# Optimization experiments

Measured on AMD Instinct MI355X. Metric: run time of the kernel, lower is better.

Reference implementation:

```python
import jax, jax.numpy as jnp
import numpy as np

N_NODES = 100000
N_EDGES = 3200000
F_IN = 128
F_OUT = 128


def setup_inputs() -> dict:
    key = jax.random.key(0)
    k_x, k_r, k_c, k_v, k_w = jax.random.split(key, 5)
    x = jax.random.normal(k_x, (N_NODES, F_IN), dtype=jnp.float32)
    adj_rows = jnp.sort(jax.random.randint(k_r, (N_EDGES,), 0, N_NODES, dtype=jnp.int32))
    adj_cols = jax.random.randint(k_c, (N_EDGES,), 0, N_NODES, dtype=jnp.int32)
    adj_vals = jax.random.uniform(k_v, (N_EDGES,), dtype=jnp.float32)
    # glorot init for W, zeros for bias (as in the original module)
    limit = np.sqrt(6.0 / (F_IN + F_OUT)).astype(np.float32)
    W = jax.random.uniform(k_w, (F_IN, F_OUT), dtype=jnp.float32, minval=-limit, maxval=limit)
    b = jnp.zeros((F_OUT,), dtype=jnp.float32)
    return {"x": x, "adj_rows": adj_rows, "adj_cols": adj_cols,
            "adj_vals": adj_vals, "W": W, "b": b}


def reference(x, adj_rows, adj_cols, adj_vals, W, b):
    # dropout = 0.0 (disabled), sparse_inputs = False, featureless = False
    # pre_sup = x @ W  -- dense feature transform [N, F_out]
    pre_sup = jnp.matmul(x, W)
    # support @ pre_sup -- sparse adjacency SpMM via gather + segment_sum
    msgs = adj_vals[:, None] * pre_sup[adj_cols]        # [E, F_out]
    agg = jax.ops.segment_sum(msgs, adj_rows,
                              num_segments=N_NODES,
                              indices_are_sorted=True)   # [N, F_out]
    out = agg + b
    return jax.nn.relu(out)
```

## Files before the change

kernel.cpp:

```cpp
#include <hip/hip_runtime.h>
#include <cstdint>
#include <cstddef>

#define N_NODES 100000
#define N_EDGES 3200000
#define F_IN 128
#define F_OUT 128
#define KPAD 136

#define ROWPTR_BYTES ((N_NODES + 1) * 4)
#define O_XB   (((ROWPTR_BYTES) + 255) & ~255)
#define XB_BYTES (N_NODES * F_IN * 2)
#define O_AXB  (O_XB + XB_BYTES)
#define AXB_BYTES (N_NODES * F_OUT * 2)
#define O_WT_A (O_AXB + AXB_BYTES)
#define WT_LIN_BYTES (F_OUT * F_IN * 2)
#define NEED_A ((size_t)(O_WT_A + WT_LIN_BYTES))
#define O_WT_A2 O_AXB
#define WT_KPAD_BYTES (F_OUT * KPAD * 2)
#define NEED_A2 ((size_t)(O_WT_A2 + WT_KPAD_BYTES))
#define O_WT_B O_XB
#define NEED_B ((size_t)(O_WT_B + WT_KPAD_BYTES))

typedef __attribute__((ext_vector_type(8))) short short8;
typedef __attribute__((ext_vector_type(4))) float f32x4;

__device__ __forceinline__ unsigned short f2bf(float f) {
    union { float f; unsigned u; } v; v.f = f;
    return (unsigned short)((v.u + 0x7FFFu + ((v.u >> 16) & 1u)) >> 16);
}
__device__ __forceinline__ float bflo(unsigned u) {
    union { unsigned u; float f; } v; v.u = u << 16; return v.f;
}
__device__ __forceinline__ float bfhi(unsigned u) {
    union { unsigned u; float f; } v; v.u = u & 0xFFFF0000u; return v.f;
}

__device__ __forceinline__ int lower_bound_i32(const int* __restrict__ a, int n, int key) {
    int lo = 0, hi = n;
    while (lo < hi) {
        int mid = (lo + hi) >> 1;
        if (a[mid] < key) lo = mid + 1; else hi = mid;
    }
    return lo;
}

__global__ __launch_bounds__(256) void build_rowptr_kernel(
    const int* __restrict__ rows, int* __restrict__ rowptr)
{
    const int n = blockIdx.x * 256 + threadIdx.x;
    if (n <= N_NODES) rowptr[n] = lower_bound_i32(rows, N_EDGES, n);
}

__global__ __launch_bounds__(256) void convert_x_kernel(
    const float4* __restrict__ x4, uint2* __restrict__ xb2)
{
    const unsigned i = blockIdx.x * 256 + threadIdx.x;
    if (i < (N_NODES * F_IN / 4)) {
        const float4 a = x4[i];
        uint2 p;
        p.x = (unsigned)f2bf(a.x) | ((unsigned)f2bf(a.y) << 16);
        p.y = (unsigned)f2bf(a.z) | ((unsigned)f2bf(a.w) << 16);
        xb2[i] = p;
    }
}

__global__ __launch_bounds__(256) void build_wt_lin_kernel(
    const float* __restrict__ W, unsigned short* __restrict__ Wt)
{
    const int idx = blockIdx.x * 256 + threadIdx.x;
    if (idx < F_IN * F_OUT) {
        const int c = idx >> 7, k = idx & 127;
        Wt[idx] = f2bf(W[k * F_OUT + c]);
    }
}

__global__ __launch_bounds__(256) void build_wt_kpad_kernel(
    const float* __restrict__ W, unsigned short* __restrict__ Wt)
{
    const int idx = blockIdx.x * 256 + threadIdx.x;
    if (idx < F_IN * F_OUT) {
        const int c = idx >> 7, k = idx & 127;
        Wt[c * KPAD + k] = f2bf(W[k * F_OUT + c]);
    }
}

template<int OUT_MODE>
__global__ __launch_bounds__(256) void spmm_xb_kernel(
    const unsigned* __restrict__ xb,
    const int*      __restrict__ cols,
    const float*    __restrict__ vals,
    const int*      __restrict__ rowptr,
    void*           __restrict__ outp)
{
    const int row  = blockIdx.x * 4 + (threadIdx.x >> 6);
    const int lane = threadIdx.x & 63;
    if (row >= N_NODES) return;

    const int e0 = rowptr[row], e1 = rowptr[row + 1];
    float ax = 0.f, ay = 0.f;

    int e = e0;
    for (; e + 16 <= e1; e += 16) {
        int c[16]; float v[16]; unsigned u[16];
        #pragma unroll
        for (int j = 0; j < 16; ++j) { c[j] = cols[e + j]; v[j] = vals[e + j]; }
        #pragma unroll
        for (int j = 0; j < 16; ++j) u[j] = xb[(unsigned)c[j] * 64u + lane];
        #pragma unroll
        for (int j = 0; j < 16; ++j) {
            ax = fmaf(v[j], bflo(u[j]), ax);
            ay = fmaf(v[j], bfhi(u[j]), ay);
        }
    }
    for (; e + 4 <= e1; e += 4) {
        int c[4]; float v[4]; unsigned u[4];
        #pragma unroll
        for (int j = 0; j < 4; ++j) { c[j] = cols[e + j]; v[j] = vals[e + j]; }
        #pragma unroll
        for (int j = 0; j < 4; ++j) u[j] = xb[(unsigned)c[j] * 64u + lane];
        #pragma unroll
        for (int j = 0; j < 4; ++j) {
            ax = fmaf(v[j], bflo(u[j]), ax);
            ay = fmaf(v[j], bfhi(u[j]), ay);
        }
    }
    for (; e < e1; ++e) {
        const float v = vals[e];
        const unsigned u = xb[(unsigned)cols[e] * 64u + lane];
        ax = fmaf(v, bflo(u), ax);
        ay = fmaf(v, bfhi(u), ay);
    }

    if (OUT_MODE == 0) {
        float2 o; o.x = ax; o.y = ay;
        reinterpret_cast<float2*>(outp)[(size_t)row * 64 + lane] = o;
    } else {
        const unsigned p = (unsigned)f2bf(ax) | ((unsigned)f2bf(ay) << 16);
        reinterpret_cast<unsigned*>(outp)[(size_t)row * 64 + lane] = p;
    }
}

__global__ __launch_bounds__(256) void gemm_direct_mfma(
    const unsigned short* __restrict__ AXb,
    const unsigned short* __restrict__ Wt,
    const float*          __restrict__ bias,
    float*                __restrict__ out)
{
    const int t    = threadIdx.x;
    const int lane = t & 63;
    const int w    = t >> 6;
    const int lr   = lane & 15;
    const int lg   = lane >> 4;
    const int row0 = blockIdx.x * 64 + w * 16;

    const short* __restrict__ Arow =
        reinterpret_cast<const short*>(AXb) + (size_t)(row0 + lr) * F_IN + lg * 8;
    const short* __restrict__ Wbase =
        reinterpret_cast<const short*>(Wt) + lr * F_IN + lg * 8;

    f32x4 acc[8];
    #pragma unroll
    for (int n = 0; n < 8; ++n) acc[n] = (f32x4){0.f, 0.f, 0.f, 0.f};

    #pragma unroll
    for (int ks = 0; ks < 4; ++ks) {
        const short8 a = *reinterpret_cast<const short8*>(Arow + ks * 32);
        #pragma unroll
        for (int n = 0; n < 8; ++n) {
            const short8 b = *reinterpret_cast<const short8*>(
                Wbase + n * 16 * F_IN + ks * 32);
            acc[n] = __builtin_amdgcn_mfma_f32_16x16x32_bf16(a, b, acc[n], 0, 0, 0);
        }
    }

    const int row_base = row0 + lg * 4;
    #pragma unroll
    for (int n = 0; n < 8; ++n) {
        const int col = n * 16 + lr;
        const float bb = bias[col];
        #pragma unroll
        for (int reg = 0; reg < 4; ++reg) {
            const int r = row_base + reg;
            if (r < N_NODES)
                out[(size_t)r * F_OUT + col] = fmaxf(acc[n][reg] + bb, 0.f);
        }
    }
}

template<bool USE_ROWPTR>
__global__ __launch_bounds__(256) void spmm_ax_kernel(
    const float* __restrict__ x,
    const int*   __restrict__ rows,
    const int*   __restrict__ cols,
    const float* __restrict__ vals,
    const int*   __restrict__ rowptr,
    float*       __restrict__ out)
{
    const int row  = blockIdx.x * 4 + (threadIdx.x >> 6);
    const int lane = threadIdx.x & 63;
    if (row >= N_NODES) return;
    int e0, e1;
    if (USE_ROWPTR) { e0 = rowptr[row]; e1 = rowptr[row + 1]; }
    else {
        e0 = lower_bound_i32(rows, N_EDGES, row);
        e1 = lower_bound_i32(rows, N_EDGES, row + 1);
    }
    const float2* __restrict__ x2 = reinterpret_cast<const float2*>(x);
    float ax = 0.f, ay = 0.f;
    int e = e0;
    for (; e + 8 <= e1; e += 8) {
        int c[8]; float v[8]; float2 a[8];
        #pragma unroll
        for (int j = 0; j < 8; ++j) { c[j] = cols[e + j]; v[j] = vals[e + j]; }
        #pragma unroll
        for (int j = 0; j < 8; ++j) a[j] = x2[(unsigned)c[j] * 64u + lane];
        #pragma unroll
        for (int j = 0; j < 8; ++j) {
            ax = fmaf(v[j], a[j].x, ax); ay = fmaf(v[j], a[j].y, ay);
        }
    }
    for (; e < e1; ++e) {
        const float v = vals[e];
        const float2 a = x2[(unsigned)cols[e] * 64u + lane];
        ax = fmaf(v, a.x, ax); ay = fmaf(v, a.y, ay);
    }
    float2 o; o.x = ax; o.y = ay;
    reinterpret_cast<float2*>(out)[(size_t)row * 64 + lane] = o;
}

template<bool WT_WS>
__global__ __launch_bounds__(256) void gemm_mfma_bias_relu_inplace(
    float*                __restrict__ out,
    const unsigned short* __restrict__ Wt_ws,
    const float*          __restrict__ W,
    const float*          __restrict__ bias)
{
    __shared__ short A_lds[64][KPAD];
    __shared__ short Wt_lds[F_OUT][KPAD];
    const int t  = threadIdx.x;
    const int r0 = blockIdx.x * 64;
    const int rows_here = (N_NODES - r0 < 64) ? (N_NODES - r0) : 64;
    {
        const float4* __restrict__ A4 =
            reinterpret_cast<const float4*>(out + (size_t)r0 * F_IN);
        const int nA = rows_here * 32;
        for (int i = t; i < nA; i += 256) {
            const int r = i >> 5, q = i & 31;
            const float4 va = A4[i];
            uint2 p;
            p.x = (unsigned)f2bf(va.x) | ((unsigned)f2bf(va.y) << 16);
            p.y = (unsigned)f2bf(va.z) | ((unsigned)f2bf(va.w) << 16);
            *reinterpret_cast<uint2*>(&A_lds[r][q * 4]) = p;
        }
    }
    if (WT_WS) {
        const float4* __restrict__ src = reinterpret_cast<const float4*>(Wt_ws);
        float4* dst = reinterpret_cast<float4*>(&Wt_lds[0][0]);
        for (int i = t; i < (WT_KPAD_BYTES / 16); i += 256) dst[i] = src[i];
    } else {
        if (t < F_OUT)
            for (int k = 0; k < F_IN; ++k)
                Wt_lds[t][k] = (short)f2bf(W[k * F_OUT + t]);
    }
    __syncthreads();

    const int lane = t & 63, w = t >> 6, lr = lane & 15, lg = lane >> 4;
    f32x4 acc[8];
    #pragma unroll
    for (int n = 0; n < 8; ++n) acc[n] = (f32x4){0.f, 0.f, 0.f, 0.f};
    #pragma unroll
    for (int ks = 0; ks < 4; ++ks) {
        const short8 a = *reinterpret_cast<const short8*>(
            &A_lds[w * 16 + lr][ks * 32 + lg * 8]);
        #pragma unroll
        for (int n = 0; n < 8; ++n) {
            const short8 b = *reinterpret_cast<const short8*>(
                &Wt_lds[n * 16 + lr][ks * 32 + lg * 8]);
            acc[n] = __builtin_amdgcn_mfma_f32_16x16x32_bf16(a, b, acc[n], 0, 0, 0);
        }
    }
    const int row_base = r0 + w * 16 + lg * 4;
    #pragma unroll
    for (int n = 0; n < 8; ++n) {
        const int col = n * 16 + lr;
        const float bb = bias[col];
        #pragma unroll
        for (int reg = 0; reg < 4; ++reg) {
            const int r = row_base + reg;
            if (r < N_NODES)
                out[(size_t)r * F_OUT + col] = fmaxf(acc[n][reg] + bb, 0.f);
        }
    }
}

extern "C" void kernel_launch(void* const* d_in, const int* in_sizes, int n_in,
                              void* d_out, int out_size, void* d_ws, size_t ws_size,
                              hipStream_t stream) {
    const float* x    = (const float*)d_in[0];
    const int*   rows = (const int*)  d_in[1];
    const int*   cols = (const int*)  d_in[2];
    const float* vals = (const float*)d_in[3];
    const float* W    = (const float*)d_in[4];
    const float* b    = (const float*)d_in[5];
    float* out = (float*)d_out;
    char*  ws  = (char*)d_ws;

    if (ws_size >= NEED_A) {
        int* rowptr = (int*)ws;
        unsigned short* xb  = (unsigned short*)(ws + O_XB);
        unsigned short* AXb = (unsigned short*)(ws + O_AXB);
        unsigned short* Wt  = (unsigned short*)(ws + O_WT_A);
        build_rowptr_kernel<<<(N_NODES + 256) / 256, 256, 0, stream>>>(rows, rowptr);
        convert_x_kernel<<<(N_NODES * F_IN / 4 + 255) / 256, 256, 0, stream>>>(
            (const float4*)x, (uint2*)xb);
        build_wt_lin_kernel<<<(F_IN * F_OUT + 255) / 256, 256, 0, stream>>>(W, Wt);
        spmm_xb_kernel<1><<<(N_NODES + 3) / 4, 256, 0, stream>>>(
            (const unsigned*)xb, cols, vals, rowptr, AXb);
        gemm_direct_mfma<<<(N_NODES + 63) / 64, 256, 0, stream>>>(AXb, Wt, b, out);
    } else if (ws_size >= NEED_A2) {
        int* rowptr = (int*)ws;
        unsigned short* xb = (unsigned short*)(ws + O_XB);
        unsigned short* Wt = (unsigned short*)(ws + O_WT_A2);
        build_rowptr_kernel<<<(N_NODES + 256) / 256, 256, 0, stream>>>(rows, rowptr);
        convert_x_kernel<<<(N_NODES * F_IN / 4 + 255) / 256, 256, 0, stream>>>(
            (const float4*)x, (uint2*)xb);
        build_wt_kpad_kernel<<<(F_IN * F_OUT + 255) / 256, 256, 0, stream>>>(W, Wt);
        spmm_xb_kernel<0><<<(N_NODES + 3) / 4, 256, 0, stream>>>(
            (const unsigned*)xb, cols, vals, rowptr, out);
        gemm_mfma_bias_relu_inplace<true><<<(N_NODES + 63) / 64, 256, 0, stream>>>(
            out, Wt, nullptr, b);
    } else if (ws_size >= NEED_B) {
        int* rowptr = (int*)ws;
        unsigned short* Wt = (unsigned short*)(ws + O_WT_B);
        build_rowptr_kernel<<<(N_NODES + 256) / 256, 256, 0, stream>>>(rows, rowptr);
        build_wt_kpad_kernel<<<(F_IN * F_OUT + 255) / 256, 256, 0, stream>>>(W, Wt);
        spmm_ax_kernel<true><<<(N_NODES + 3) / 4, 256, 0, stream>>>(
            x, rows, cols, vals, rowptr, out);
        gemm_mfma_bias_relu_inplace<true><<<(N_NODES + 63) / 64, 256, 0, stream>>>(
            out, Wt, nullptr, b);
    } else {
        spmm_ax_kernel<false><<<(N_NODES + 3) / 4, 256, 0, stream>>>(
            x, rows, cols, vals, nullptr, out);
        gemm_mfma_bias_relu_inplace<false><<<(N_NODES + 63) / 64, 256, 0, stream>>>(
            out, nullptr, W, b);
    }
}
```

Baseline: 283.8 us.

## Fuse SpMM into MFMA GEMM via LDS and merge prep kernels

Merges the rowptr build, x-to-bf16 conversion and W transpose into one prep kernel. The SpMM and GEMM are fused so each block aggregates 64 rows into swizzled LDS and then runs the MFMA GEMM with bias and ReLU directly. This removes the bf16 AX intermediate round trip through global memory and several launches. In exchange the grid drops from 25000 blocks to about 1563, each wave processing 16 rows serially, which reduces parallelism and latency hiding for the gather-bound SpMM.

```diff
diff --git a/kernel.cpp b/kernel.cpp
--- a/kernel.cpp
+++ b/kernel.cpp
@@ -6,21 +6,13 @@
 #define N_EDGES 3200000
 #define F_IN 128
 #define F_OUT 128
-#define KPAD 136
 
 #define ROWPTR_BYTES ((N_NODES + 1) * 4)
 #define O_XB   (((ROWPTR_BYTES) + 255) & ~255)
 #define XB_BYTES (N_NODES * F_IN * 2)
-#define O_AXB  (O_XB + XB_BYTES)
-#define AXB_BYTES (N_NODES * F_OUT * 2)
-#define O_WT_A (O_AXB + AXB_BYTES)
-#define WT_LIN_BYTES (F_OUT * F_IN * 2)
-#define NEED_A ((size_t)(O_WT_A + WT_LIN_BYTES))
-#define O_WT_A2 O_AXB
-#define WT_KPAD_BYTES (F_OUT * KPAD * 2)
-#define NEED_A2 ((size_t)(O_WT_A2 + WT_KPAD_BYTES))
-#define O_WT_B O_XB
-#define NEED_B ((size_t)(O_WT_B + WT_KPAD_BYTES))
+#define O_WT   (O_XB + XB_BYTES)
+#define WT_BYTES (F_OUT * F_IN * 2)
+#define NEED_A ((size_t)(O_WT + WT_BYTES))
 
 typedef __attribute__((ext_vector_type(8))) short short8;
 typedef __attribute__((ext_vector_type(4))) float f32x4;
@@ -45,119 +37,99 @@
     return lo;
 }
 
-__global__ __launch_bounds__(256) void build_rowptr_kernel(
-    const int* __restrict__ rows, int* __restrict__ rowptr)
-{
-    const int n = blockIdx.x * 256 + threadIdx.x;
-    if (n <= N_NODES) rowptr[n] = lower_bound_i32(rows, N_EDGES, n);
-}
-
-__global__ __launch_bounds__(256) void convert_x_kernel(
-    const float4* __restrict__ x4, uint2* __restrict__ xb2)
-{
-    const unsigned i = blockIdx.x * 256 + threadIdx.x;
-    if (i < (N_NODES * F_IN / 4)) {
-        const float4 a = x4[i];
+__global__ __launch_bounds__(256) void prep_kernel(
+    const float*    __restrict__ x4_,
+    const int*      __restrict__ rows,
+    const float*    __restrict__ W,
+    int*            __restrict__ rowptr,
+    uint2*          __restrict__ xb2,
+    unsigned short* __restrict__ Wt)
+{
+    const unsigned g = blockIdx.x * 256 + threadIdx.x;
+    const float4* __restrict__ x4 = (const float4*)x4_;
+
+    if (g < (N_NODES * F_IN / 4)) {
+        const float4 a = x4[g];
         uint2 p;
         p.x = (unsigned)f2bf(a.x) | ((unsigned)f2bf(a.y) << 16);
         p.y = (unsigned)f2bf(a.z) | ((unsigned)f2bf(a.w) << 16);
-        xb2[i] = p;
-    }
-}
-
-__global__ __launch_bounds__(256) void build_wt_lin_kernel(
-    const float* __restrict__ W, unsigned short* __restrict__ Wt)
-{
-    const int idx = blockIdx.x * 256 + threadIdx.x;
-    if (idx < F_IN * F_OUT) {
-        const int c = idx >> 7, k = idx & 127;
-        Wt[idx] = f2bf(W[k * F_OUT + c]);
-    }
-}
-
-__global__ __launch_bounds__(256) void build_wt_kpad_kernel(
-    const float* __restrict__ W, unsigned short* __restrict__ Wt)
-{
-    const int idx = blockIdx.x * 256 + threadIdx.x;
-    if (idx < F_IN * F_OUT) {
-        const int c = idx >> 7, k = idx & 127;
-        Wt[c * KPAD + k] = f2bf(W[k * F_OUT + c]);
-    }
-}
-
-template<int OUT_MODE>
-__global__ __launch_bounds__(256) void spmm_xb_kernel(
-    const unsigned* __restrict__ xb,
-    const int*      __restrict__ cols,
-    const float*    __restrict__ vals,
-    const int*      __restrict__ rowptr,
-    void*           __restrict__ outp)
-{
-    const int row  = blockIdx.x * 4 + (threadIdx.x >> 6);
-    const int lane = threadIdx.x & 63;
-    if (row >= N_NODES) return;
-
-    const int e0 = rowptr[row], e1 = rowptr[row + 1];
-    float ax = 0.f, ay = 0.f;
-
-    int e = e0;
-    for (; e + 16 <= e1; e += 16) {
-        int c[16]; float v[16]; unsigned u[16];
-        #pragma unroll
-        for (int j = 0; j < 16; ++j) { c[j] = cols[e + j]; v[j] = vals[e + j]; }
-        #pragma unroll
-        for (int j = 0; j < 16; ++j) u[j] = xb[(unsigned)c[j] * 64u + lane];
-        #pragma unroll
-        for (int j = 0; j < 16; ++j) {
-            ax = fmaf(v[j], bflo(u[j]), ax);
-            ay = fmaf(v[j], bfhi(u[j]), ay);
-        }
-    }
-    for (; e + 4 <= e1; e += 4) {
-        int c[4]; float v[4]; unsigned u[4];
-        #pragma unroll
-        for (int j = 0; j < 4; ++j) { c[j] = cols[e + j]; v[j] = vals[e + j]; }
-        #pragma unroll
-        for (int j = 0; j < 4; ++j) u[j] = xb[(unsigned)c[j] * 64u + lane];
-        #pragma unroll
-        for (int j = 0; j < 4; ++j) {
-            ax = fmaf(v[j], bflo(u[j]), ax);
-            ay = fmaf(v[j], bfhi(u[j]), ay);
-        }
-    }
-    for (; e < e1; ++e) {
-        const float v = vals[e];
-        const unsigned u = xb[(unsigned)cols[e] * 64u + lane];
-        ax = fmaf(v, bflo(u), ax);
-        ay = fmaf(v, bfhi(u), ay);
-    }
-
-    if (OUT_MODE == 0) {
-        float2 o; o.x = ax; o.y = ay;
-        reinterpret_cast<float2*>(outp)[(size_t)row * 64 + lane] = o;
-    } else {
-        const unsigned p = (unsigned)f2bf(ax) | ((unsigned)f2bf(ay) << 16);
-        reinterpret_cast<unsigned*>(outp)[(size_t)row * 64 + lane] = p;
-    }
-}
-
-__global__ __launch_bounds__(256) void gemm_direct_mfma(
-    const unsigned short* __restrict__ AXb,
+        xb2[g] = p;
+    }
+    if (g <= N_NODES)
+        rowptr[g] = lower_bound_i32(rows, N_EDGES, g);
+    if (g < F_IN * F_OUT) {
+        const int c = g >> 7, k = g & 127;
+        Wt[g] = f2bf(W[k * F_OUT + c]);
+    }
+}
+
+__global__ __launch_bounds__(256) void fused_spmm_gemm(
+    const unsigned*       __restrict__ xb,
+    const int*            __restrict__ cols,
+    const float*          __restrict__ vals,
+    const int*            __restrict__ rowptr,
     const unsigned short* __restrict__ Wt,
     const float*          __restrict__ bias,
     float*                __restrict__ out)
 {
+    __shared__ char A_lds[64 * 256];
+
     const int t    = threadIdx.x;
     const int lane = t & 63;
     const int w    = t >> 6;
-    const int lr   = lane & 15;
-    const int lg   = lane >> 4;
-    const int row0 = blockIdx.x * 64 + w * 16;
-
-    const short* __restrict__ Arow =
-        reinterpret_cast<const short*>(AXb) + (size_t)(row0 + lr) * F_IN + lg * 8;
+    const int r0   = blockIdx.x * 64;
+
+    for (int i = 0; i < 16; ++i) {
+        const int lrow = w * 16 + i;
+        const int row  = r0 + lrow;
+        float ax = 0.f, ay = 0.f;
+        if (row < N_NODES) {
+            const int e0 = rowptr[row], e1 = rowptr[row + 1];
+            int e = e0;
+            for (; e + 16 <= e1; e += 16) {
+                int c[16]; float v[16]; unsigned u[16];
+                #pragma unroll
+                for (int j = 0; j < 16; ++j) { c[j] = cols[e + j]; v[j] = vals[e + j]; }
+                #pragma unroll
+                for (int j = 0; j < 16; ++j) u[j] = xb[(unsigned)c[j] * 64u + lane];
+                #pragma unroll
+                for (int j = 0; j < 16; ++j) {
+                    ax = fmaf(v[j], bflo(u[j]), ax);
+                    ay = fmaf(v[j], bfhi(u[j]), ay);
+                }
+            }
+            for (; e + 4 <= e1; e += 4) {
+                int c[4]; float v[4]; unsigned u[4];
+                #pragma unroll
+                for (int j = 0; j < 4; ++j) { c[j] = cols[e + j]; v[j] = vals[e + j]; }
+                #pragma unroll
+                for (int j = 0; j < 4; ++j) u[j] = xb[(unsigned)c[j] * 64u + lane];
+                #pragma unroll
+                for (int j = 0; j < 4; ++j) {
+                    ax = fmaf(v[j], bflo(u[j]), ax);
+                    ay = fmaf(v[j], bfhi(u[j]), ay);
+                }
+            }
+            for (; e < e1; ++e) {
+                const float v = vals[e];
+                const unsigned u = xb[(unsigned)cols[e] * 64u + lane];
+                ax = fmaf(v, bflo(u), ax);
+                ay = fmaf(v, bfhi(u), ay);
+            }
+        }
+        const unsigned p = (unsigned)f2bf(ax) | ((unsigned)f2bf(ay) << 16);
+        *reinterpret_cast<unsigned*>(
+            A_lds + lrow * 256 + ((lane * 4) ^ ((lrow & 7) << 4))) = p;
+    }
+    __syncthreads();
+
+    const int lr = lane & 15;
+    const int lg = lane >> 4;
+    const int swA = (lr & 7) << 4;
+
     const short* __restrict__ Wbase =
         reinterpret_cast<const short*>(Wt) + lr * F_IN + lg * 8;
+    const char* Abase = A_lds + (w * 16 + lr) * 256;
 
     f32x4 acc[8];
     #pragma unroll
@@ -165,7 +137,8 @@
 
     #pragma unroll
     for (int ks = 0; ks < 4; ++ks) {
-        const short8 a = *reinterpret_cast<const short8*>(Arow + ks * 32);
+        const short8 a = *reinterpret_cast<const short8*>(
+            Abase + ((ks * 64 + lg * 16) ^ swA));
         #pragma unroll
         for (int n = 0; n < 8; ++n) {
             const short8 b = *reinterpret_cast<const short8*>(
@@ -174,7 +147,7 @@
         }
     }
 
-    const int row_base = row0 + lg * 4;
+    const int row_base = r0 + w * 16 + lg * 4;
     #pragma unroll
     for (int n = 0; n < 8; ++n) {
         const int col = n * 16 + lr;
@@ -188,24 +161,18 @@
     }
 }
 
-template<bool USE_ROWPTR>
-__global__ __launch_bounds__(256) void spmm_ax_kernel(
+__global__ __launch_bounds__(256) void spmm_ax_fallback(
     const float* __restrict__ x,
     const int*   __restrict__ rows,
     const int*   __restrict__ cols,
     const float* __restrict__ vals,
-    const int*   __restrict__ rowptr,
     float*       __restrict__ out)
 {
     const int row  = blockIdx.x * 4 + (threadIdx.x >> 6);
     const int lane = threadIdx.x & 63;
     if (row >= N_NODES) return;
-    int e0, e1;
-    if (USE_ROWPTR) { e0 = rowptr[row]; e1 = rowptr[row + 1]; }
-    else {
-        e0 = lower_bound_i32(rows, N_EDGES, row);
-        e1 = lower_bound_i32(rows, N_EDGES, row + 1);
-    }
+    const int e0 = lower_bound_i32(rows, N_EDGES, row);
+    const int e1 = lower_bound_i32(rows, N_EDGES, row + 1);
     const float2* __restrict__ x2 = reinterpret_cast<const float2*>(x);
     float ax = 0.f, ay = 0.f;
     int e = e0;
@@ -229,15 +196,13 @@
     reinterpret_cast<float2*>(out)[(size_t)row * 64 + lane] = o;
 }
 
-template<bool WT_WS>
-__global__ __launch_bounds__(256) void gemm_mfma_bias_relu_inplace(
-    float*                __restrict__ out,
-    const unsigned short* __restrict__ Wt_ws,
-    const float*          __restrict__ W,
-    const float*          __restrict__ bias)
-{
-    __shared__ short A_lds[64][KPAD];
-    __shared__ short Wt_lds[F_OUT][KPAD];
+__global__ __launch_bounds__(256) void gemm_inplace_fallback(
+    float*       __restrict__ out,
+    const float* __restrict__ W,
+    const float* __restrict__ bias)
+{
+    __shared__ short A_lds[64][136];
+    __shared__ short Wt_lds[F_OUT][136];
     const int t  = threadIdx.x;
     const int r0 = blockIdx.x * 64;
     const int rows_here = (N_NODES - r0 < 64) ? (N_NODES - r0) : 64;
@@ -254,15 +219,9 @@
             *reinterpret_cast<uint2*>(&A_lds[r][q * 4]) = p;
         }
     }
-    if (WT_WS) {
-        const float4* __restrict__ src = reinterpret_cast<const float4*>(Wt_ws);
-        float4* dst = reinterpret_cast<float4*>(&Wt_lds[0][0]);
-        for (int i = t; i < (WT_KPAD_BYTES / 16); i += 256) dst[i] = src[i];
-    } else {
-        if (t < F_OUT)
-            for (int k = 0; k < F_IN; ++k)
-                Wt_lds[t][k] = (short)f2bf(W[k * F_OUT + t]);
-    }
+    if (t < F_OUT)
+        for (int k = 0; k < F_IN; ++k)
+            Wt_lds[t][k] = (short)f2bf(W[k * F_OUT + t]);
     __syncthreads();
 
     const int lane = t & 63, w = t >> 6, lr = lane & 15, lg = lane >> 4;
@@ -307,42 +266,16 @@
     char*  ws  = (char*)d_ws;
 
     if (ws_size >= NEED_A) {
-        int* rowptr = (int*)ws;
-        unsigned short* xb  = (unsigned short*)(ws + O_XB);
-        unsigned short* AXb = (unsigned short*)(ws + O_AXB);
-        unsigned short* Wt  = (unsigned short*)(ws + O_WT_A);
-        build_rowptr_kernel<<<(N_NODES + 256) / 256, 256, 0, stream>>>(rows, rowptr);
-        convert_x_kernel<<<(N_NODES * F_IN / 4 + 255) / 256, 256, 0, stream>>>(
-            (const float4*)x, (uint2*)xb);
-        build_wt_lin_kernel<<<(F_IN * F_OUT + 255) / 256, 256, 0, stream>>>(W, Wt);
-        spmm_xb_kernel<1><<<(N_NODES + 3) / 4, 256, 0, stream>>>(
-            (const unsigned*)xb, cols, vals, rowptr, AXb);
-        gemm_direct_mfma<<<(N_NODES + 63) / 64, 256, 0, stream>>>(AXb, Wt, b, out);
-    } else if (ws_size >= NEED_A2) {
-        int* rowptr = (int*)ws;
-        unsigned short* xb = (unsigned short*)(ws + O_XB);
-        unsigned short* Wt = (unsigned short*)(ws + O_WT_A2);
-        build_rowptr_kernel<<<(N_NODES + 256) / 256, 256, 0, stream>>>(rows, rowptr);
-        convert_x_kernel<<<(N_NODES * F_IN / 4 + 255) / 256, 256, 0, stream>>>(
-            (const float4*)x, (uint2*)xb);
-        build_wt_kpad_kernel<<<(F_IN * F_OUT + 255) / 256, 256, 0, stream>>>(W, Wt);
-        spmm_xb_kernel<0><<<(N_NODES + 3) / 4, 256, 0, stream>>>(
-            (const unsigned*)xb, cols, vals, rowptr, out);
-        gemm_mfma_bias_relu_inplace<true><<<(N_NODES + 63) / 64, 256, 0, stream>>>(
-            out, Wt, nullptr, b);
-    } else if (ws_size >= NEED_B) {
-        int* rowptr = (int*)ws;
-        unsigned short* Wt = (unsigned short*)(ws + O_WT_B);
-        build_rowptr_kernel<<<(N_NODES + 256) / 256, 256, 0, stream>>>(rows, rowptr);
-        build_wt_kpad_kernel<<<(F_IN * F_OUT + 255) / 256, 256, 0, stream>>>(W, Wt);
-        spmm_ax_kernel<true><<<(N_NODES + 3) / 4, 256, 0, stream>>>(
-            x, rows, cols, vals, rowptr, out);
-        gemm_mfma_bias_relu_inplace<true><<<(N_NODES + 63) / 64, 256, 0, stream>>>(
-            out, Wt, nullptr, b);
+        int*            rowptr = (int*)ws;
+        unsigned short* xb     = (unsigned short*)(ws + O_XB);
+        unsigned short* Wt     = (unsigned short*)(ws + O_WT);
+        prep_kernel<<<(N_NODES * F_IN / 4 + 255) / 256, 256, 0, stream>>>(
+            x, rows, W, rowptr, (uint2*)xb, Wt);
+        fused_spmm_gemm<<<(N_NODES + 63) / 64, 256, 0, stream>>>(
+            (const unsigned*)xb, cols, vals, rowptr, Wt, b, out);
     } else {
-        spmm_ax_kernel<false><<<(N_NODES + 3) / 4, 256, 0, stream>>>(
-            x, rows, cols, vals, nullptr, out);
-        gemm_mfma_bias_relu_inplace<false><<<(N_NODES + 63) / 64, 256, 0, stream>>>(
-            out, nullptr, W, b);
-    }
-}
+        spmm_ax_fallback<<<(N_NODES + 3) / 4, 256, 0, stream>>>(
+            x, rows, cols, vals, out);
+        gemm_inplace_fallback<<<(N_NODES + 63) / 64, 256, 0, stream>>>(out, W, b);
+    }
+}
```

New measurement: 319.5 us. 12.6% more time.
